# Performance work log

Measured on AMD Instinct MI355X. Metric: run time of the kernel, lower is better.

The kernel has to match this reference:

```python
import jax, jax.numpy as jnp
import numpy as np

MARGIN = 0.1
N, CHOICES = 16384, 2048


def setup_inputs() -> dict:
    key = jax.random.key(0)
    k1, k2 = jax.random.split(key)
    cossim = jax.random.normal(k1, (N, CHOICES), dtype=jnp.float32)
    correct_idx = jax.random.randint(k2, (N,), 0, CHOICES)
    # one-hot int64 target: exactly one 1 per row, as the module expects
    target = (jnp.arange(CHOICES)[None, :] == correct_idx[:, None]).astype(jnp.int64)
    return {"cossim": cossim, "target": target}


def reference(cossim, target):
    # correct index / similarity per row
    correct_idx = jnp.argmax(target, axis=1)                                   # [N]
    correct_sim = jnp.take_along_axis(cossim, correct_idx[:, None], axis=1)    # [N,1]
    # hinge over all choices, then zero out the correct-choice term
    hinge = jnp.maximum(MARGIN + cossim - correct_sim, 0.0)                    # [N,C]
    hinge = jnp.where(target == 1, 0.0, hinge)
    loss = jnp.sum(hinge, axis=1)                                              # [N]
    return jnp.mean(loss)
```

## Files before the change

### kernel.cpp

```cpp
#include <hip/hip_runtime.h>
#include <hip/hip_bf16.h>


constexpr int   kC      = 2048;
constexpr float kMargin = 0.1f;
constexpr int   kBatch  = 8;

__global__ __launch_bounds__(256) void find_correct_sim(
    const float* __restrict__ cossim,
    const int4*  __restrict__ target4,
    float*       __restrict__ csim)
{
    const int tid = threadIdx.x;
    const size_t blockBase = (size_t)blockIdx.x * (kBatch * 256);

    int4 v[kBatch];
    #pragma unroll
    for (int k = 0; k < kBatch; ++k)
        v[k] = target4[blockBase + k * 256 + tid];

    #pragma unroll
    for (int k = 0; k < kBatch; ++k) {
        int4 t = v[k];
        if ((t.x | t.y | t.z | t.w) != 0) {
            size_t f   = blockBase + k * 256 + tid;
            size_t e   = f * 4;
            int    row = (int)(e >> 11);
            int    col = (int)(e & (kC - 1));
            const float* cr = cossim + ((size_t)row << 11);
            float s = t.x ? cr[col]     :
                      t.y ? cr[col + 1] :
                      t.z ? cr[col + 2] : cr[col + 3];
            csim[row] = s;
        }
    }
}

__global__ __launch_bounds__(256) void hinge_sum(
    const float4* __restrict__ cossim4,
    const float*  __restrict__ csim,
    float*        __restrict__ out,
    float inv_n)
{
    const int tid = threadIdx.x;
    const size_t blockBase = (size_t)blockIdx.x * (kBatch * 256);

    float4 v[kBatch];
    float  sim[kBatch];
    #pragma unroll
    for (int k = 0; k < kBatch; ++k) {
        size_t f = blockBase + k * 256 + tid;
        v[k]   = cossim4[f];
        sim[k] = csim[f >> 9];
    }

    float s = 0.0f;
    #pragma unroll
    for (int k = 0; k < kBatch; ++k) {
        float m = kMargin - sim[k];
        s += fmaxf(m + v[k].x, 0.0f);
        s += fmaxf(m + v[k].y, 0.0f);
        s += fmaxf(m + v[k].z, 0.0f);
        s += fmaxf(m + v[k].w, 0.0f);
    }

    #pragma unroll
    for (int o = 32; o > 0; o >>= 1)
        s += __shfl_xor(s, o);

    __shared__ float ws[4];
    const int lane = tid & 63;
    const int wib  = tid >> 6;
    if (lane == 0) ws[wib] = s;
    __syncthreads();
    if (tid == 0) {
        float b   = ws[0] + ws[1] + ws[2] + ws[3];
        float add = b * inv_n;
        if (blockIdx.x == 0) add -= kMargin;
        atomicAdd(out, add);
    }
}

extern "C" void kernel_launch(void* const* d_in, const int* in_sizes, int n_in,
                              void* d_out, int out_size, void* d_ws, size_t ws_size,
                              hipStream_t stream)
{
    const float* cossim = (const float*)d_in[0];
    const int*   target = (const int*)d_in[1];
    float*       out    = (float*)d_out;
    float*       csim   = (float*)d_ws;

    const int nrows  = in_sizes[0] / kC;
    const int total4 = in_sizes[1] / 4;
    const int blocksA = total4 / (kBatch * 256);
    const int blocksB = (in_sizes[0] / 4) / (kBatch * 256);

    hipMemsetAsync(out, 0, sizeof(float), stream);

    find_correct_sim<<<blocksA, 256, 0, stream>>>(cossim, (const int4*)target, csim);
    hinge_sum<<<blocksB, 256, 0, stream>>>((const float4*)cossim, csim, out,
                                           1.0f / (float)nrows);
}
```

Measured before the change: 289.1 us.

## Fuse correct-sim lookup and hinge sum into one pass with partial reduction

Merges the two kernels into one. Each block loads the target and cossim tiles together, picks the correct similarity for its 4 rows from registers into shared memory, and computes the hinge sum without a global scratch array. The memset and the per-block float atomics are replaced by per-block partials and a single-block final reduction kernel. This drops a launch and the scattered csim write/read, at the cost of an extra barrier and a small tail kernel.

```diff
diff --git a/kernel.cpp b/kernel.cpp
--- a/kernel.cpp
+++ b/kernel.cpp
@@ -6,62 +6,42 @@
 constexpr float kMargin = 0.1f;
 constexpr int   kBatch  = 8;
 
-__global__ __launch_bounds__(256) void find_correct_sim(
-    const float* __restrict__ cossim,
-    const int4*  __restrict__ target4,
-    float*       __restrict__ csim)
+__global__ __launch_bounds__(256) void max_margin_main(
+    const float4* __restrict__ cossim4,
+    const int4*   __restrict__ target4,
+    float*        __restrict__ partials)
 {
     const int tid = threadIdx.x;
-    const size_t blockBase = (size_t)blockIdx.x * (kBatch * 256);
+    const size_t base = (size_t)blockIdx.x * (kBatch * 256);
 
-    int4 v[kBatch];
-    #pragma unroll
-    for (int k = 0; k < kBatch; ++k)
-        v[k] = target4[blockBase + k * 256 + tid];
-
+    int4   t[kBatch];
+    float4 c[kBatch];
     #pragma unroll
     for (int k = 0; k < kBatch; ++k) {
-        int4 t = v[k];
-        if ((t.x | t.y | t.z | t.w) != 0) {
-            size_t f   = blockBase + k * 256 + tid;
-            size_t e   = f * 4;
-            int    row = (int)(e >> 11);
-            int    col = (int)(e & (kC - 1));
-            const float* cr = cossim + ((size_t)row << 11);
-            float s = t.x ? cr[col]     :
-                      t.y ? cr[col + 1] :
-                      t.z ? cr[col + 2] : cr[col + 3];
-            csim[row] = s;
+        size_t g = base + k * 256 + tid;
+        t[k] = target4[g];
+        c[k] = cossim4[g];
+    }
+
+    __shared__ float s_sim[4];
+    #pragma unroll
+    for (int k = 0; k < kBatch; ++k) {
+        if ((t[k].x | t[k].y | t[k].z | t[k].w) != 0) {
+            float v = t[k].x ? c[k].x : (t[k].y ? c[k].y
+                    : (t[k].z ? c[k].z : c[k].w));
+            s_sim[k >> 1] = v;
         }
     }
-}
-
-__global__ __launch_bounds__(256) void hinge_sum(
-    const float4* __restrict__ cossim4,
-    const float*  __restrict__ csim,
-    float*        __restrict__ out,
-    float inv_n)
-{
-    const int tid = threadIdx.x;
-    const size_t blockBase = (size_t)blockIdx.x * (kBatch * 256);
-
-    float4 v[kBatch];
-    float  sim[kBatch];
-    #pragma unroll
-    for (int k = 0; k < kBatch; ++k) {
-        size_t f = blockBase + k * 256 + tid;
-        v[k]   = cossim4[f];
-        sim[k] = csim[f >> 9];
-    }
+    __syncthreads();
 
     float s = 0.0f;
     #pragma unroll
     for (int k = 0; k < kBatch; ++k) {
-        float m = kMargin - sim[k];
-        s += fmaxf(m + v[k].x, 0.0f);
-        s += fmaxf(m + v[k].y, 0.0f);
-        s += fmaxf(m + v[k].z, 0.0f);
-        s += fmaxf(m + v[k].w, 0.0f);
+        float m = kMargin - s_sim[k >> 1];
+        s += fmaxf(m + c[k].x, 0.0f);
+        s += fmaxf(m + c[k].y, 0.0f);
+        s += fmaxf(m + c[k].z, 0.0f);
+        s += fmaxf(m + c[k].w, 0.0f);
     }
 
     #pragma unroll
@@ -73,12 +53,31 @@
     const int wib  = tid >> 6;
     if (lane == 0) ws[wib] = s;
     __syncthreads();
-    if (tid == 0) {
-        float b   = ws[0] + ws[1] + ws[2] + ws[3];
-        float add = b * inv_n;
-        if (blockIdx.x == 0) add -= kMargin;
-        atomicAdd(out, add);
-    }
+    if (tid == 0)
+        partials[blockIdx.x] = ws[0] + ws[1] + ws[2] + ws[3];
+}
+
+__global__ __launch_bounds__(256) void final_reduce(
+    const float* __restrict__ partials,
+    float*       __restrict__ out,
+    int nparts, float inv_n)
+{
+    const int tid = threadIdx.x;
+    float s = 0.0f;
+    for (int i = tid; i < nparts; i += 256)
+        s += partials[i];
+
+    #pragma unroll
+    for (int o = 32; o > 0; o >>= 1)
+        s += __shfl_xor(s, o);
+
+    __shared__ float ws[4];
+    const int lane = tid & 63;
+    const int wib  = tid >> 6;
+    if (lane == 0) ws[wib] = s;
+    __syncthreads();
+    if (tid == 0)
+        out[0] = (ws[0] + ws[1] + ws[2] + ws[3]) * inv_n - kMargin;
 }
 
 extern "C" void kernel_launch(void* const* d_in, const int* in_sizes, int n_in,
@@ -88,16 +87,13 @@
     const float* cossim = (const float*)d_in[0];
     const int*   target = (const int*)d_in[1];
     float*       out    = (float*)d_out;
-    float*       csim   = (float*)d_ws;
+    float*       parts  = (float*)d_ws;
 
     const int nrows  = in_sizes[0] / kC;
-    const int total4 = in_sizes[1] / 4;
-    const int blocksA = total4 / (kBatch * 256);
-    const int blocksB = (in_sizes[0] / 4) / (kBatch * 256);
+    const int blocks = in_sizes[0] / (kBatch * 256 * 4);
 
-    hipMemsetAsync(out, 0, sizeof(float), stream);
-
-    find_correct_sim<<<blocksA, 256, 0, stream>>>(cossim, (const int4*)target, csim);
-    hinge_sum<<<blocksB, 256, 0, stream>>>((const float4*)cossim, csim, out,
-                                           1.0f / (float)nrows);
+    max_margin_main<<<blocks, 256, 0, stream>>>(
+        (const float4*)cossim, (const int4*)target, parts);
+    final_reduce<<<1, 256, 0, stream>>>(parts, out, blocks,
+                                        1.0f / (float)nrows);
 }
```

Result: faster. 278.6 us (-3.6%).
